# Optimization experiments

Measured on AMD Instinct MI355X. Metric: run time of the kernel, lower is better.

Reference implementation:

```python
import jax, jax.numpy as jnp
import numpy as np

EPS = 1e-5
M = 8          # num_modules
NUM_LAYERS = 4


def gumbel_softmax(logits, u, tau):
    g = -jnp.log(-jnp.log(jnp.clip(u, 1e-10, 1.0 - 1e-7)))
    return jax.nn.softmax((logits + g) / tau, axis=-1)


def batchnorm(x, gamma, beta):
    # training-mode BN over batch axis 0; x: [B, ...], gamma/beta broadcast over trailing dims
    mean = jnp.mean(x, axis=0, keepdims=True)
    var = jnp.mean(jnp.square(x - mean), axis=0, keepdims=True)  # biased var, as torch BN
    return (x - mean) * jax.lax.rsqrt(var + EPS) * gamma + beta


def setup_inputs() -> dict:
    key = jax.random.key(0)
    ks = jax.random.split(key, 32)
    B = 16384
    d = {}
    d['x'] = jax.random.normal(ks[0], (B, 128), jnp.float32)
    d['embedding_input'] = jax.random.normal(ks[1], (B, 128), jnp.float32)
    d['u_sel'] = jax.random.uniform(ks[2], (B, NUM_LAYERS - 1, M, M), jnp.float32)
    d['u_final'] = jax.random.uniform(ks[3], (B, M), jnp.float32)
    shapes = [('base_W0', (128, 400)), ('base_b0', (400,)), ('base_W1', (400, 256)), ('base_b1', (256,)),
              ('em_W0', (128, 400)), ('em_b0', (400,)),
              ('gat_W0', (400, 256)), ('gat_b0', (256,)), ('gat_W1', (256, 256)), ('gat_b1', (256,)),
              ('sel_W', (3, 256, 64)), ('sel_b', (3, 64)), ('selF_W', (256, 8)), ('selF_b', (8,)),
              ('cond_W', (3, 64, 256)), ('cond_b', (3, 256)),
              ('mod_W', (8, 256, 256)), ('mod_b', (8, 256)),
              ('last_W', (256, 18)), ('last_b', (18,))]
    for i, (name, sh) in enumerate(shapes):
        fan_in = sh[-2] if len(sh) >= 2 else sh[-1]
        d[name] = jax.random.normal(ks[4 + i], sh, jnp.float32) / np.sqrt(fan_in)
    d['bn1_g'] = jnp.ones((8, 256), jnp.float32)
    d['bn1_b'] = jnp.zeros((8, 256), jnp.float32)
    d['bn2_g'] = jnp.ones((8, 256), jnp.float32)
    d['bn2_b'] = jnp.zeros((8, 256), jnp.float32)
    return d


def forward(x, embedding_input, u_sel, u_final,
            base_W0, base_b0, base_W1, base_b1, em_W0, em_b0,
            gat_W0, gat_b0, gat_W1, gat_b1,
            sel_W, sel_b, selF_W, selF_b, cond_W, cond_b,
            mod_W, mod_b, bn1_g, bn1_b, bn2_g, bn2_b, last_W, last_b):
    relu = jax.nn.relu
    # base MLP (last activation is identity)
    h = relu(x @ base_W0 + base_b0)
    out = h @ base_W1 + base_b1                       # [B, 256]
    # embedding base (single layer, identity last activation)
    emb = embedding_input @ em_W0 + em_b0             # [B, 400]
    # gating fcs: activation THEN fc, per source loop
    emb = relu(emb) @ gat_W0 + gat_b0
    emb = relu(emb) @ gat_W1 + gat_b1                 # [B, 256]

    # routing logits (stochastic branch, tau = select_temp = 1.0)
    select_input = relu(emb)
    gsels = []
    for i in range(NUM_LAYERS - 1):
        logit = jnp.tanh(select_input @ sel_W[i] + sel_b[i])       # [B, 64]
        sraw = logit.reshape(logit.shape[0], M, M)                  # [B, M, M]
        gsels.append(gumbel_softmax(sraw, u_sel[:, i], 1.0))
        select_input = relu((logit @ cond_W[i] + cond_b[i]) * emb)
    final_select = gumbel_softmax(select_input @ selF_W + selF_b, u_final, 1.0)  # [B, M]
    # selects were insert(0, ...)'d in torch -> consumed in reversed order
    selects = gsels[::-1]

    # layer-0 expert modules: BN -> Linear -> BN (only layers[0] is used in forward)
    mean = jnp.mean(out, axis=0, keepdims=True)
    var = jnp.mean(jnp.square(out - mean), axis=0, keepdims=True)
    xhat = (out - mean) * jax.lax.rsqrt(var + EPS)                  # shared normalization
    t = xhat[:, None, :] * bn1_g + bn1_b                            # [B, M, 256] per-module affine
    h = jnp.einsum('bmd,mdh->bmh', t, mod_W) + mod_b                # [B, M, 256]
    prev = batchnorm(h, bn2_g, bn2_b)                               # [B, M, 256]

    # cascade: weighted combination + relu per layer
    for l in range(NUM_LAYERS - 1):
        prev = relu(jnp.einsum('bmk,bkh->bmh', selects[l], prev))
    out = jnp.einsum('bm,bmh->bh', final_select, prev)              # [B, 256]
    return out @ last_W + last_b                                    # [B, 18]


def reference(x, embedding_input, u_sel, u_final,
              base_W0, base_b0, base_W1, base_b1, em_W0, em_b0,
              gat_W0, gat_b0, gat_W1, gat_b1,
              sel_W, sel_b, selF_W, selF_b, cond_W, cond_b,
              mod_W, mod_b, bn1_g, bn1_b, bn2_g, bn2_b, last_W, last_b):
    return forward(x, embedding_input, u_sel, u_final,
                   base_W0, base_b0, base_W1, base_b1, em_W0, em_b0,
                   gat_W0, gat_b0, gat_W1, gat_b1,
                   sel_W, sel_b, selF_W, selF_b, cond_W, cond_b,
                   mod_W, mod_b, bn1_g, bn1_b, bn2_g, bn2_b, last_W, last_b)
```

## Files before the change

kernel.cpp:

```cpp
#include <hip/hip_runtime.h>
#include <math.h>


typedef short bf16x8 __attribute__((ext_vector_type(8)));
typedef float f32x4 __attribute__((ext_vector_type(4)));

__device__ __forceinline__ unsigned short f2bf(float f) {
  unsigned u = __float_as_uint(f);
  u += 0x7fffu + ((u >> 16) & 1u);
  return (unsigned short)(u >> 16);
}
__device__ __forceinline__ float bf2f(unsigned short h) {
  return __uint_as_float(((unsigned)h) << 16);
}
__device__ __forceinline__ unsigned pack2(float a, float b) {
  return ((unsigned)f2bf(b) << 16) | f2bf(a);
}
__device__ __forceinline__ void gload_lds16(const void* g, void* l) {
  __builtin_amdgcn_global_load_lds(
      (const __attribute__((address_space(1))) unsigned int*)g,
      (__attribute__((address_space(3))) unsigned int*)l, 16, 0, 0);
}
__device__ __forceinline__ bf16x8 relu_bf8(bf16x8 v) {
  bf16x8 r;
  #pragma unroll
  for (int j = 0; j < 8; ++j) r[j] = v[j] > 0 ? v[j] : (short)0;
  return r;
}

#define EPI_NONE  0
#define EPI_RELU  1
#define EPI_STATS 4

__global__ __launch_bounds__(256) void prep_all(
    const float* __restrict__ base_W0, const float* __restrict__ em_W0,
    const float* __restrict__ base_W1, const float* __restrict__ gat_W0,
    const float* __restrict__ gat_W1, const float* __restrict__ sel_W,
    const float* __restrict__ cond_W, const float* __restrict__ last_W,
    const float* __restrict__ selF_W,
    unsigned short* __restrict__ W0t, unsigned short* __restrict__ emW0t,
    unsigned short* __restrict__ W1t, unsigned short* __restrict__ g0t,
    unsigned short* __restrict__ g1t, unsigned short* __restrict__ selWt,
    unsigned short* __restrict__ condWt, unsigned short* __restrict__ lastWt,
    unsigned short* __restrict__ selFt, float* __restrict__ stats)
{
  __shared__ float t[32][33];
  int bid = blockIdx.x;
  const int tid = threadIdx.x;
  const int tx = tid & 31, ty = tid >> 5;

  if (bid < 496) {
    const float* src; unsigned short* dst; int K, N, KP, gx, local;
    if (bid < 64)       { src = base_W0; dst = W0t;   K = 128; N = 400; KP = 128; gx = 4;  local = bid; }
    else if (bid < 128) { src = em_W0;   dst = emW0t; K = 128; N = 400; KP = 128; gx = 4;  local = bid - 64; }
    else if (bid < 232) { src = base_W1; dst = W1t;   K = 400; N = 256; KP = 416; gx = 13; local = bid - 128; }
    else if (bid < 336) { src = gat_W0;  dst = g0t;   K = 400; N = 256; KP = 416; gx = 13; local = bid - 232; }
    else if (bid < 400) { src = gat_W1;  dst = g1t;   K = 256; N = 256; KP = 256; gx = 8;  local = bid - 336; }
    else if (bid < 448) {
      const int i = (bid - 400) / 16;
      src = sel_W + i * 16384; dst = selWt + i * 16384;
      K = 256; N = 64; KP = 256; gx = 8; local = (bid - 400) % 16;
    } else {
      const int i = (bid - 448) / 16;
      src = cond_W + i * 16384; dst = condWt + i * 16384;
      K = 64; N = 256; KP = 64; gx = 2; local = (bid - 448) % 16;
    }
    const int k0 = (local % gx) * 32, n0 = (local / gx) * 32;
    #pragma unroll
    for (int p = 0; p < 4; ++p) {
      const int k = k0 + ty + p * 8;
      t[ty + p * 8][tx] = (k < K && n0 + tx < N) ? src[(size_t)k * N + n0 + tx] : 0.f;
    }
    __syncthreads();
    #pragma unroll
    for (int p = 0; p < 4; ++p) {
      const int n = n0 + ty + p * 8;
      dst[(size_t)n * KP + k0 + tx] = f2bf(t[tx][ty + p * 8]);
    }
    return;
  }
  bid -= 496;

  if (bid < 8) {
    const int k0 = bid * 32;
    #pragma unroll
    for (int p = 0; p < 4; ++p)
      t[ty + p * 8][tx] = (tx < 18) ? last_W[(size_t)(k0 + ty + p * 8) * 18 + tx] : 0.f;
    __syncthreads();
    #pragma unroll
    for (int p = 0; p < 4; ++p) {
      const int n = ty + p * 8;
      lastWt[(size_t)n * 256 + k0 + tx] = f2bf(t[tx][n]);
      lastWt[(size_t)(n + 32) * 256 + k0 + tx] = 0;
    }
    return;
  }
  bid -= 8;

  if (bid == 0) {
    const int k = tid;
    #pragma unroll
    for (int j = 0; j < 8; ++j) selFt[j * 256 + k] = f2bf(selF_W[k * 8 + j]);
    #pragma unroll
    for (int j = 8; j < 16; ++j) selFt[j * 256 + k] = 0;
    return;
  }

  for (int i = tid; i < 4608; i += 256) stats[i] = 0.f;
}

__global__ __launch_bounds__(256) void gemm_w0(
    const float* __restrict__ Ax, const float* __restrict__ Ae,
    const unsigned short* __restrict__ Wx, const unsigned short* __restrict__ We,
    const float* __restrict__ bx, const float* __restrict__ be,
    unsigned short* __restrict__ Cx, unsigned short* __restrict__ Ce)
{
  __shared__ unsigned short As[128 * 32];
  __shared__ unsigned short Bs[128 * 32];
  const float* Ap = blockIdx.z ? Ae : Ax;
  const unsigned short* Wp = blockIdx.z ? We : Wx;
  const float* bp = blockIdx.z ? be : bx;
  unsigned short* Cp = blockIdx.z ? Ce : Cx;
  const int row0 = blockIdx.y * 128;
  const int n0 = blockIdx.x * 128;
  const int tid = threadIdx.x;
  const int wid = tid >> 6, lane = tid & 63;
  const int wr = wid >> 1, wc = wid & 1;
  const int arow = tid >> 2, kcol = (tid & 3) * 8;
  const int lr = lane & 15, lk = (lane >> 4) * 8;
  const int lrow = (lane >> 4) * 4;

  f32x4 acc[4][4] = {};
  for (int k0 = 0; k0 < 128; k0 += 32) {
    {
      const float4* s1 = reinterpret_cast<const float4*>(
          Ap + (size_t)(row0 + arow) * 128 + k0 + kcol);
      uint4 w1 = {pack2(s1[0].x, s1[0].y), pack2(s1[0].z, s1[0].w),
                  pack2(s1[1].x, s1[1].y), pack2(s1[1].z, s1[1].w)};
      *reinterpret_cast<uint4*>(&As[arow * 32 + kcol]) = w1;
      const float4* s2 = reinterpret_cast<const float4*>(
          Ap + (size_t)(row0 + 64 + arow) * 128 + k0 + kcol);
      uint4 w2 = {pack2(s2[0].x, s2[0].y), pack2(s2[0].z, s2[0].w),
                  pack2(s2[1].x, s2[1].y), pack2(s2[1].z, s2[1].w)};
      *reinterpret_cast<uint4*>(&As[(64 + arow) * 32 + kcol]) = w2;
    }
    gload_lds16(Wp + (size_t)(n0 + arow) * 128 + k0 + kcol, (char*)Bs + tid * 16);
    gload_lds16(Wp + (size_t)(n0 + 64 + arow) * 128 + k0 + kcol,
                (char*)Bs + 4096 + tid * 16);
    __syncthreads();
    bf16x8 a[4], b[4];
    #pragma unroll
    for (int i = 0; i < 4; ++i)
      a[i] = *reinterpret_cast<const bf16x8*>(&As[(wr * 64 + i * 16 + lr) * 32 + lk]);
    #pragma unroll
    for (int j = 0; j < 4; ++j)
      b[j] = *reinterpret_cast<const bf16x8*>(&Bs[(wc * 64 + j * 16 + lr) * 32 + lk]);
    #pragma unroll
    for (int i = 0; i < 4; ++i)
      #pragma unroll
      for (int j = 0; j < 4; ++j)
        acc[i][j] = __builtin_amdgcn_mfma_f32_16x16x32_bf16(a[i], b[j], acc[i][j], 0, 0, 0);
    __syncthreads();
  }
  #pragma unroll
  for (int j = 0; j < 4; ++j) {
    const int col = n0 + wc * 64 + j * 16 + lr;
    if (col >= 416) continue;
    const bool real = col < 400;
    const float bv = real ? bp[col] : 0.f;
    #pragma unroll
    for (int i = 0; i < 4; ++i) {
      #pragma unroll
      for (int r = 0; r < 4; ++r) {
        const int row = row0 + wr * 64 + i * 16 + lrow + r;
        float v = real ? fmaxf(acc[i][j][r] + bv, 0.f) : 0.f;
        Cp[(size_t)row * 416 + col] = f2bf(v);
      }
    }
  }
}

__global__ __launch_bounds__(256) void gemm_mid(
    const unsigned short* __restrict__ A0, const unsigned short* __restrict__ W0,
    const float* __restrict__ b0, unsigned short* __restrict__ C0,
    const unsigned short* __restrict__ A1, const unsigned short* __restrict__ W1,
    const float* __restrict__ b1, unsigned short* __restrict__ C1,
    float* __restrict__ sum, float* __restrict__ sumsq)
{
  __shared__ unsigned short As[128 * 32];
  __shared__ unsigned short Bs[64 * 32];
  const bool z1 = blockIdx.z != 0;
  const unsigned short* A = z1 ? A1 : A0;
  const unsigned short* Wt = z1 ? W1 : W0;
  const float* bias = z1 ? b1 : b0;
  unsigned short* C = z1 ? C1 : C0;
  const int row0 = blockIdx.y * 128;
  const int n0 = blockIdx.x * 64;
  const int tid = threadIdx.x;
  const int wid = tid >> 6, lane = tid & 63;
  const int arow = tid >> 2, kcol = (tid & 3) * 8;
  const int lr = lane & 15, lk = (lane >> 4) * 8;
  const int lrow = (lane >> 4) * 4;

  f32x4 acc[2][4] = {};
  for (int k0 = 0; k0 < 416; k0 += 32) {
    gload_lds16(A + (size_t)(row0 + arow) * 416 + k0 + kcol, (char*)As + tid * 16);
    gload_lds16(A + (size_t)(row0 + 64 + arow) * 416 + k0 + kcol, (char*)As + 4096 + tid * 16);
    gload_lds16(Wt + (size_t)(n0 + arow) * 416 + k0 + kcol, (char*)Bs + tid * 16);
    __syncthreads();
    bf16x8 a[2], b[4];
    #pragma unroll
    for (int i = 0; i < 2; ++i)
      a[i] = *reinterpret_cast<const bf16x8*>(&As[(wid * 32 + i * 16 + lr) * 32 + lk]);
    #pragma unroll
    for (int j = 0; j < 4; ++j)
      b[j] = *reinterpret_cast<const bf16x8*>(&Bs[(j * 16 + lr) * 32 + lk]);
    #pragma unroll
    for (int i = 0; i < 2; ++i)
      #pragma unroll
      for (int j = 0; j < 4; ++j)
        acc[i][j] = __builtin_amdgcn_mfma_f32_16x16x32_bf16(a[i], b[j], acc[i][j], 0, 0, 0);
    __syncthreads();
  }
  #pragma unroll
  for (int j = 0; j < 4; ++j) {
    const int col = n0 + j * 16 + lr;
    const float bv = bias[col];
    float s = 0.f, q = 0.f;
    #pragma unroll
    for (int i = 0; i < 2; ++i) {
      #pragma unroll
      for (int r = 0; r < 4; ++r) {
        const int row = row0 + wid * 32 + i * 16 + lrow + r;
        float v = acc[i][j][r] + bv;
        if (z1) v = fmaxf(v, 0.f);
        const unsigned short hv = f2bf(v);
        C[(size_t)row * 256 + col] = hv;
        if (!z1) {
          const float vr = bf2f(hv);
          s += vr;
          q = fmaf(vr, vr, q);
        }
      }
    }
    if (!z1) {
      s += __shfl_xor(s, 16); s += __shfl_xor(s, 32);
      q += __shfl_xor(q, 16); q += __shfl_xor(q, 32);
      if (lane < 16) {
        atomicAdd(&sum[col], s);
        atomicAdd(&sumsq[col], q);
      }
    }
  }
}

template<int BN, int WM, int WN, int EPI, bool RELU_A>
__global__ __launch_bounds__(256) void gemm_bf16(
    const unsigned short* __restrict__ A, int AS,
    const unsigned short* __restrict__ Wt, const float* __restrict__ bias,
    unsigned short* __restrict__ C, int CS, int Nreal, int NP, int K,
    const unsigned short* __restrict__ emb,
    float* __restrict__ sum, float* __restrict__ sumsq)
{
  constexpr int FRAG_M = 128 / WM / 16;
  constexpr int FRAG_N = BN / WN / 16;
  __shared__ unsigned short As[128 * 32];
  __shared__ unsigned short Bs[BN * 32];
  const int row0 = blockIdx.y * 128;
  const int n0 = blockIdx.x * BN;
  const int tid = threadIdx.x;
  const int wid = tid >> 6, lane = tid & 63;
  const int wr = wid / WN, wc = wid % WN;
  const int arow = tid >> 2;
  const int kcol = (tid & 3) * 8;
  const int lr = lane & 15, lk = (lane >> 4) * 8;
  const int lrow = (lane >> 4) * 4;

  f32x4 acc[FRAG_M][FRAG_N] = {};
  for (int k0 = 0; k0 < K; k0 += 32) {
    gload_lds16(A + (size_t)(row0 + arow) * AS + k0 + kcol, (char*)As + tid * 16);
    gload_lds16(A + (size_t)(row0 + 64 + arow) * AS + k0 + kcol, (char*)As + 4096 + tid * 16);
    gload_lds16(Wt + (size_t)(n0 + arow) * K + k0 + kcol, (char*)Bs + tid * 16);
    if constexpr (BN == 128)
      gload_lds16(Wt + (size_t)(n0 + 64 + arow) * K + k0 + kcol, (char*)Bs + 4096 + tid * 16);
    __syncthreads();
    bf16x8 a[FRAG_M], b[FRAG_N];
    #pragma unroll
    for (int i = 0; i < FRAG_M; ++i) {
      a[i] = *reinterpret_cast<const bf16x8*>(&As[(wr * (128 / WM) + i * 16 + lr) * 32 + lk]);
      if (RELU_A) a[i] = relu_bf8(a[i]);
    }
    #pragma unroll
    for (int j = 0; j < FRAG_N; ++j)
      b[j] = *reinterpret_cast<const bf16x8*>(&Bs[(wc * (BN / WN) + j * 16 + lr) * 32 + lk]);
    #pragma unroll
    for (int i = 0; i < FRAG_M; ++i)
      #pragma unroll
      for (int j = 0; j < FRAG_N; ++j)
        acc[i][j] = __builtin_amdgcn_mfma_f32_16x16x32_bf16(a[i], b[j], acc[i][j], 0, 0, 0);
    __syncthreads();
  }
  #pragma unroll
  for (int j = 0; j < FRAG_N; ++j) {
    const int col = n0 + wc * (BN / WN) + j * 16 + lr;
    if (col >= NP) continue;
    const bool real = col < Nreal;
    const float bv = real ? bias[col] : 0.f;
    float s = 0.f, q = 0.f;
    #pragma unroll
    for (int i = 0; i < FRAG_M; ++i) {
      #pragma unroll
      for (int r = 0; r < 4; ++r) {
        const int row = row0 + wr * (128 / WM) + i * 16 + lrow + r;
        float v = acc[i][j][r] + bv;
        if (EPI == EPI_RELU) v = fmaxf(v, 0.f);
        if (!real) v = 0.f;
        const unsigned short hv = f2bf(v);
        C[(size_t)row * CS + col] = hv;
        if (EPI == EPI_STATS) {
          const float vr = bf2f(hv);
          s += vr;
          q = fmaf(vr, vr, q);
        }
      }
    }
    if (EPI == EPI_STATS) {
      s += __shfl_xor(s, 16); s += __shfl_xor(s, 32);
      q += __shfl_xor(q, 16); q += __shfl_xor(q, 32);
      if (lane < 16) {
        atomicAdd(&sum[col], s);
        atomicAdd(&sumsq[col], q);
      }
    }
  }
}

__global__ __launch_bounds__(256) void gemm_mod(
    const unsigned short* __restrict__ A,
    const unsigned short* __restrict__ Wt,
    const float* __restrict__ bias, unsigned short* __restrict__ C,
    float* __restrict__ sum, float* __restrict__ sumsq)
{
  __shared__ unsigned short As[128 * 32];
  __shared__ unsigned short Bs[128 * 32];
  const int lin = blockIdx.x;
  const int swz = (lin & 7) * 256 + (lin >> 3);
  const int row0 = (swz >> 4) * 128;
  const int n0 = (swz & 15) * 128;
  const int tid = threadIdx.x;
  const int wid = tid >> 6, lane = tid & 63;
  const int wr = wid >> 1, wc = wid & 1;
  const int arow = tid >> 2;
  const int kcol = (tid & 3) * 8;
  const int lr = lane & 15, lk = (lane >> 4) * 8;
  const int lrow = (lane >> 4) * 4;

  f32x4 acc[4][4] = {};
  for (int k0 = 0; k0 < 256; k0 += 32) {
    gload_lds16(A + (size_t)(row0 + arow) * 256 + k0 + kcol, (char*)As + tid * 16);
    gload_lds16(A + (size_t)(row0 + 64 + arow) * 256 + k0 + kcol, (char*)As + 4096 + tid * 16);
    gload_lds16(Wt + (size_t)(n0 + arow) * 256 + k0 + kcol, (char*)Bs + tid * 16);
    gload_lds16(Wt + (size_t)(n0 + 64 + arow) * 256 + k0 + kcol, (char*)Bs + 4096 + tid * 16);
    __syncthreads();
    bf16x8 a[4], b[4];
    #pragma unroll
    for (int i = 0; i < 4; ++i)
      a[i] = *reinterpret_cast<const bf16x8*>(&As[(wr * 64 + i * 16 + lr) * 32 + lk]);
    #pragma unroll
    for (int j = 0; j < 4; ++j)
      b[j] = *reinterpret_cast<const bf16x8*>(&Bs[(wc * 64 + j * 16 + lr) * 32 + lk]);
    #pragma unroll
    for (int i = 0; i < 4; ++i)
      #pragma unroll
      for (int j = 0; j < 4; ++j)
        acc[i][j] = __builtin_amdgcn_mfma_f32_16x16x32_bf16(a[i], b[j], acc[i][j], 0, 0, 0);
    __syncthreads();
  }
  #pragma unroll
  for (int j = 0; j < 4; ++j) {
    const int col = n0 + wc * 64 + j * 16 + lr;
    const float bv = bias[col];
    float s = 0.f, q = 0.f;
    #pragma unroll
    for (int i = 0; i < 4; ++i) {
      #pragma unroll
      for (int r = 0; r < 4; ++r) {
        const int row = row0 + wr * 64 + i * 16 + lrow + r;
        const unsigned short hv = f2bf(acc[i][j][r] + bv);
        C[(size_t)row * 2048 + col] = hv;
        const float vr = bf2f(hv);
        s += vr;
        q = fmaf(vr, vr, q);
      }
    }
    s += __shfl_xor(s, 16); s += __shfl_xor(s, 32);
    q += __shfl_xor(q, 16); q += __shfl_xor(q, 32);
    if (lane < 16) {
      atomicAdd(&sum[col], s);
      atomicAdd(&sumsq[col], q);
    }
  }
}

template<bool RELU_A>
__global__ __launch_bounds__(256) void fused_select(
    const unsigned short* __restrict__ A, const unsigned short* __restrict__ selWt,
    const float* __restrict__ selb, const unsigned short* __restrict__ condWt,
    const float* __restrict__ condb, const unsigned short* __restrict__ emb,
    const float* __restrict__ u, int u_off,
    float* __restrict__ gs, unsigned short* __restrict__ siout)
{
  __shared__ unsigned short As[128 * 32];
  __shared__ unsigned short Bs[64 * 32];
  __shared__ unsigned short Ls[128 * 72];
  const int tid = threadIdx.x;
  const int wid = tid >> 6, lane = tid & 63;
  const int lr = lane & 15, hi = lane >> 4;
  const int lk = hi * 8;
  const int row0 = blockIdx.x * 128;
  const int arow = tid >> 2, kcol = (tid & 3) * 8;

  {
    f32x4 acc[2][4] = {};
    for (int k0 = 0; k0 < 256; k0 += 32) {
      gload_lds16(A + (size_t)(row0 + arow) * 256 + k0 + kcol, (char*)As + tid * 16);
      gload_lds16(A + (size_t)(row0 + 64 + arow) * 256 + k0 + kcol, (char*)As + 4096 + tid * 16);
      gload_lds16(selWt + (size_t)arow * 256 + k0 + kcol, (char*)Bs + tid * 16);
      __syncthreads();
      bf16x8 a[2], b[4];
      #pragma unroll
      for (int i = 0; i < 2; ++i) {
        a[i] = *reinterpret_cast<const bf16x8*>(&As[(wid * 32 + i * 16 + lr) * 32 + lk]);
        if (RELU_A) a[i] = relu_bf8(a[i]);
      }
      #pragma unroll
      for (int j = 0; j < 4; ++j)
        b[j] = *reinterpret_cast<const bf16x8*>(&Bs[(j * 16 + lr) * 32 + lk]);
      #pragma unroll
      for (int i = 0; i < 2; ++i)
        #pragma unroll
        for (int j = 0; j < 4; ++j)
          acc[i][j] = __builtin_amdgcn_mfma_f32_16x16x32_bf16(a[i], b[j], acc[i][j], 0, 0, 0);
      __syncthreads();
    }
    #pragma unroll
    for (int j = 0; j < 4; ++j) {
      const int col = j * 16 + lr;
      const float bv = selb[col];
      #pragma unroll
      for (int i = 0; i < 2; ++i)
        #pragma unroll
        for (int r = 0; r < 4; ++r) {
          const int row = wid * 32 + i * 16 + hi * 4 + r;
          Ls[row * 72 + col] = f2bf(tanhf(acc[i][j][r] + bv));
        }
    }
  }
  __syncthreads();

  #pragma unroll
  for (int p = 0; p < 4; ++p) {
    const int pair = p * 256 + tid;
    const int bl = pair >> 3, mm = pair & 7;
    const int bg = row0 + bl;
    float v[8];
    #pragma unroll
    for (int jj = 0; jj < 8; ++jj) v[jj] = bf2f(Ls[bl * 72 + mm * 8 + jj]);
    const float* up = u + (size_t)bg * 192 + u_off + mm * 8;
    #pragma unroll
    for (int jj = 0; jj < 8; ++jj) {
      const float uu = fminf(fmaxf(up[jj], 1e-10f), 0.9999999f);
      v[jj] -= logf(-logf(uu));
    }
    float mx = v[0];
    #pragma unroll
    for (int jj = 1; jj < 8; ++jj) mx = fmaxf(mx, v[jj]);
    float s = 0.f;
    #pragma unroll
    for (int jj = 0; jj < 8; ++jj) { v[jj] = expf(v[jj] - mx); s += v[jj]; }
    const float inv = 1.f / s;
    float* op = gs + (size_t)bg * 64 + mm * 8;
    #pragma unroll
    for (int jj = 0; jj < 8; ++jj) op[jj] = v[jj] * inv;
  }

  {
    const int wr2 = wid >> 1, wc2 = wid & 1;
    f32x4 acc2[4][8] = {};
    #pragma unroll
    for (int kq = 0; kq < 2; ++kq) {
      const int k0 = kq * 32;
      bf16x8 a2[4];
      #pragma unroll
      for (int i = 0; i < 4; ++i)
        a2[i] = *reinterpret_cast<const bf16x8*>(
            &Ls[(wr2 * 64 + i * 16 + lr) * 72 + k0 + hi * 8]);
      #pragma unroll
      for (int j = 0; j < 8; ++j) {
        const bf16x8 b2 = *reinterpret_cast<const bf16x8*>(
            condWt + (size_t)(wc2 * 128 + j * 16 + lr) * 64 + k0 + hi * 8);
        #pragma unroll
        for (int i = 0; i < 4; ++i)
          acc2[i][j] = __builtin_amdgcn_mfma_f32_16x16x32_bf16(a2[i], b2, acc2[i][j], 0, 0, 0);
      }
    }
    #pragma unroll
    for (int j = 0; j < 8; ++j) {
      const int col = wc2 * 128 + j * 16 + lr;
      const float bv = condb[col];
      #pragma unroll
      for (int i = 0; i < 4; ++i)
        #pragma unroll
        for (int r = 0; r < 4; ++r) {
          const int row = row0 + wr2 * 64 + i * 16 + hi * 4 + r;
          float vv = (acc2[i][j][r] + bv) * bf2f(emb[(size_t)row * 256 + col]);
          siout[(size_t)row * 256 + col] = f2bf(fmaxf(vv, 0.f));
        }
    }
  }
}

__global__ __launch_bounds__(256) void gemm_fsel(
    const unsigned short* __restrict__ A, const unsigned short* __restrict__ Wt,
    const float* __restrict__ bias, const float* __restrict__ u,
    float* __restrict__ fs)
{
  __shared__ unsigned short As[128 * 32];
  __shared__ unsigned short Bs[16 * 32];
  const int row0 = blockIdx.y * 128;
  const int tid = threadIdx.x;
  const int wid = tid >> 6, lane = tid & 63;
  const int arow = tid >> 2, kcol = (tid & 3) * 8;
  const int lr = lane & 15, hi = lane >> 4;
  const int lk = hi * 8;

  f32x4 acc[2] = {};
  for (int k0 = 0; k0 < 256; k0 += 32) {
    gload_lds16(A + (size_t)(row0 + arow) * 256 + k0 + kcol, (char*)As + tid * 16);
    gload_lds16(A + (size_t)(row0 + 64 + arow) * 256 + k0 + kcol, (char*)As + 4096 + tid * 16);
    if (wid == 0)
      gload_lds16(Wt + (size_t)(lane >> 2) * 256 + k0 + (lane & 3) * 8, (char*)Bs + lane * 16);
    __syncthreads();
    bf16x8 a[2];
    #pragma unroll
    for (int i = 0; i < 2; ++i)
      a[i] = *reinterpret_cast<const bf16x8*>(&As[(wid * 32 + i * 16 + lr) * 32 + lk]);
    const bf16x8 b = *reinterpret_cast<const bf16x8*>(&Bs[lr * 32 + lk]);
    #pragma unroll
    for (int i = 0; i < 2; ++i)
      acc[i] = __builtin_amdgcn_mfma_f32_16x16x32_bf16(a[i], b, acc[i], 0, 0, 0);
    __syncthreads();
  }
  const float bv = (lr < 8) ? bias[lr] : 0.f;
  #pragma unroll
  for (int i = 0; i < 2; ++i) {
    #pragma unroll
    for (int r = 0; r < 4; ++r) {
      const int row = row0 + wid * 32 + i * 16 + hi * 4 + r;
      float v = acc[i][r] + bv;
      if (lr < 8) {
        const float uu = fminf(fmaxf(u[(size_t)row * 8 + lr], 1e-10f), 0.9999999f);
        v -= logf(-logf(uu));
      }
      float mx = v;
      mx = fmaxf(mx, __shfl_xor(mx, 1));
      mx = fmaxf(mx, __shfl_xor(mx, 2));
      mx = fmaxf(mx, __shfl_xor(mx, 4));
      const float e = expf(v - mx);
      float ssum = e;
      ssum += __shfl_xor(ssum, 1);
      ssum += __shfl_xor(ssum, 2);
      ssum += __shfl_xor(ssum, 4);
      if (lr < 8) fs[(size_t)row * 8 + lr] = e / ssum;
    }
  }
}

__global__ __launch_bounds__(256) void fold_modw_all(
    const float* __restrict__ W, const float* __restrict__ g1,
    const float* __restrict__ b1, const float* __restrict__ modb,
    const float* __restrict__ sum1, const float* __restrict__ sumsq1,
    unsigned short* __restrict__ Wt, float* __restrict__ bias2)
{
  const float invB = 1.f / 16384.f;
  if (blockIdx.z == 8) {
    if (blockIdx.y != 0) return;
    const int m = blockIdx.x, h = threadIdx.x;
    float acc = modb[m * 256 + h];
    for (int d = 0; d < 256; ++d) {
      const float mean = sum1[d] * invB;
      const float var = sumsq1[d] * invB - mean * mean;
      const float r = rsqrtf(var + 1e-5f);
      const float c = b1[m * 256 + d] - mean * r * g1[m * 256 + d];
      acc = fmaf(c, W[((size_t)m * 256 + d) * 256 + h], acc);
    }
    bias2[m * 256 + h] = acc;
    return;
  }
  __shared__ float t[32][33];
  const int m = blockIdx.z, d0 = blockIdx.y * 32, h0 = blockIdx.x * 32;
  const int tx = threadIdx.x & 31, ty = threadIdx.x >> 5;
  #pragma unroll
  for (int p = 0; p < 4; ++p) {
    const int d = d0 + ty + p * 8;
    const float mean = sum1[d] * invB;
    const float var = sumsq1[d] * invB - mean * mean;
    const float r = rsqrtf(var + 1e-5f);
    t[ty + p * 8][tx] = W[((size_t)m * 256 + d) * 256 + h0 + tx] * r * g1[m * 256 + d];
  }
  __syncthreads();
  #pragma unroll
  for (int p = 0; p < 4; ++p) {
    const int h = h0 + ty + p * 8;
    Wt[((size_t)m * 256 + h) * 256 + d0 + tx] = f2bf(t[tx][ty + p * 8]);
  }
}

__global__ void finalize_bn2(const float* __restrict__ sum, const float* __restrict__ sumsq,
                             const float* __restrict__ g, const float* __restrict__ b,
                             float* __restrict__ scale, float* __restrict__ shift)
{
  const int i = blockIdx.x * 256 + threadIdx.x;
  const float invB = 1.f / 16384.f;
  const float m = sum[i] * invB;
  const float v = sumsq[i] * invB - m * m;
  const float r = rsqrtf(v + 1e-5f);
  const float sc = r * g[i];
  scale[i] = sc;
  shift[i] = b[i] - m * sc;
}

__global__ __launch_bounds__(256) void final_cascade(
    const unsigned short* __restrict__ H, const float* __restrict__ scale2,
    const float* __restrict__ shift2, const float* __restrict__ gs0,
    const float* __restrict__ gs1, const float* __restrict__ gs2,
    const float* __restrict__ fs, unsigned short* __restrict__ ovec)
{
  const int wave = threadIdx.x >> 6, lane = threadIdx.x & 63;
  const int b = __builtin_amdgcn_readfirstlane(blockIdx.x * 4 + wave);
  const int c0 = lane << 2;

  float prev[8][4];
  #pragma unroll
  for (int m = 0; m < 8; ++m) {
    const int gc = m * 256 + c0;
    const ushort4 h = *reinterpret_cast<const ushort4*>(&H[(size_t)b * 2048 + gc]);
    const float4 sc = *reinterpret_cast<const float4*>(&scale2[gc]);
    const float4 sh = *reinterpret_cast<const float4*>(&shift2[gc]);
    prev[m][0] = bf2f(h.x) * sc.x + sh.x;
    prev[m][1] = bf2f(h.y) * sc.y + sh.y;
    prev[m][2] = bf2f(h.z) * sc.z + sh.z;
    prev[m][3] = bf2f(h.w) * sc.w + sh.w;
  }

  const float* sel0 = gs2 + (size_t)b * 64;
  const float* sel1 = gs1 + (size_t)b * 64;
  const float* sel2 = gs0 + (size_t)b * 64;
  #pragma unroll
  for (int l = 0; l < 3; ++l) {
    const float* sp = (l == 0) ? sel0 : (l == 1) ? sel1 : sel2;
    float nw[8][4];
    #pragma unroll
    for (int m = 0; m < 8; ++m) {
      float a0 = 0.f, a1 = 0.f, a2 = 0.f, a3 = 0.f;
      #pragma unroll
      for (int k = 0; k < 8; ++k) {
        const float s = sp[m * 8 + k];
        a0 = fmaf(s, prev[k][0], a0);
        a1 = fmaf(s, prev[k][1], a1);
        a2 = fmaf(s, prev[k][2], a2);
        a3 = fmaf(s, prev[k][3], a3);
      }
      nw[m][0] = fmaxf(a0, 0.f); nw[m][1] = fmaxf(a1, 0.f);
      nw[m][2] = fmaxf(a2, 0.f); nw[m][3] = fmaxf(a3, 0.f);
    }
    #pragma unroll
    for (int m = 0; m < 8; ++m)
      #pragma unroll
      for (int c = 0; c < 4; ++c)
        prev[m][c] = nw[m][c];
  }

  const float* fp = fs + (size_t)b * 8;
  float ov[4] = {0.f, 0.f, 0.f, 0.f};
  #pragma unroll
  for (int m = 0; m < 8; ++m) {
    const float s = fp[m];
    ov[0] = fmaf(s, prev[m][0], ov[0]);
    ov[1] = fmaf(s, prev[m][1], ov[1]);
    ov[2] = fmaf(s, prev[m][2], ov[2]);
    ov[3] = fmaf(s, prev[m][3], ov[3]);
  }
  ushort4 o;
  o.x = f2bf(ov[0]); o.y = f2bf(ov[1]); o.z = f2bf(ov[2]); o.w = f2bf(ov[3]);
  *reinterpret_cast<ushort4*>(&ovec[(size_t)b * 256 + c0]) = o;
}

__global__ __launch_bounds__(256) void gemm_last(
    const unsigned short* __restrict__ A, const unsigned short* __restrict__ Wt,
    const float* __restrict__ bias, float* __restrict__ out)
{
  __shared__ unsigned short As[128 * 32];
  __shared__ unsigned short Bs[64 * 32];
  const int row0 = blockIdx.y * 128;
  const int tid = threadIdx.x;
  const int wid = tid >> 6, lane = tid & 63;
  const int arow = tid >> 2;
  const int kcol = (tid & 3) * 8;
  const int lr = lane & 15, lk = (lane >> 4) * 8;
  const int lrow = (lane >> 4) * 4;

  f32x4 acc[2][4] = {};
  for (int k0 = 0; k0 < 256; k0 += 32) {
    gload_lds16(A + (size_t)(row0 + arow) * 256 + k0 + kcol, (char*)As + tid * 16);
    gload_lds16(A + (size_t)(row0 + 64 + arow) * 256 + k0 + kcol, (char*)As + 4096 + tid * 16);
    gload_lds16(Wt + (size_t)arow * 256 + k0 + kcol, (char*)Bs + tid * 16);
    __syncthreads();
    bf16x8 a[2], b[4];
    #pragma unroll
    for (int i = 0; i < 2; ++i)
      a[i] = *reinterpret_cast<const bf16x8*>(&As[(wid * 32 + i * 16 + lr) * 32 + lk]);
    #pragma unroll
    for (int j = 0; j < 4; ++j)
      b[j] = *reinterpret_cast<const bf16x8*>(&Bs[(j * 16 + lr) * 32 + lk]);
    #pragma unroll
    for (int i = 0; i < 2; ++i)
      #pragma unroll
      for (int j = 0; j < 4; ++j)
        acc[i][j] = __builtin_amdgcn_mfma_f32_16x16x32_bf16(a[i], b[j], acc[i][j], 0, 0, 0);
    __syncthreads();
  }
  #pragma unroll
  for (int j = 0; j < 2; ++j) {
    const int col = j * 16 + lr;
    if (col >= 18) continue;
    const float bv = bias[col];
    #pragma unroll
    for (int i = 0; i < 2; ++i) {
      #pragma unroll
      for (int r = 0; r < 4; ++r) {
        const int row = row0 + wid * 32 + i * 16 + lrow + r;
        out[(size_t)row * 18 + col] = acc[i][j][r] + bv;
      }
    }
  }
}

extern "C" void kernel_launch(void* const* d_in, const int* in_sizes, int n_in,
                              void* d_out, int out_size, void* d_ws, size_t ws_size,
                              hipStream_t stream)
{
  (void)in_sizes; (void)n_in; (void)out_size; (void)ws_size;
  const float* x       = (const float*)d_in[0];
  const float* embi    = (const float*)d_in[1];
  const float* u_sel   = (const float*)d_in[2];
  const float* u_fin   = (const float*)d_in[3];
  const float* base_W0 = (const float*)d_in[4];
  const float* base_b0 = (const float*)d_in[5];
  const float* base_W1 = (const float*)d_in[6];
  const float* base_b1 = (const float*)d_in[7];
  const float* em_W0   = (const float*)d_in[8];
  const float* em_b0   = (const float*)d_in[9];
  const float* gat_W0  = (const float*)d_in[10];
  const float* gat_b0  = (const float*)d_in[11];
  const float* gat_W1  = (const float*)d_in[12];
  const float* gat_b1  = (const float*)d_in[13];
  const float* sel_W   = (const float*)d_in[14];
  const float* sel_b   = (const float*)d_in[15];
  const float* selF_W  = (const float*)d_in[16];
  const float* selF_b  = (const float*)d_in[17];
  const float* cond_W  = (const float*)d_in[18];
  const float* cond_b  = (const float*)d_in[19];
  const float* mod_W   = (const float*)d_in[20];
  const float* mod_b   = (const float*)d_in[21];
  const float* last_W  = (const float*)d_in[22];
  const float* last_b  = (const float*)d_in[23];
  const float* bn1_g   = (const float*)d_in[24];
  const float* bn1_b   = (const float*)d_in[25];
  const float* bn2_g   = (const float*)d_in[26];
  const float* bn2_b   = (const float*)d_in[27];

  char* WSB = (char*)d_ws;
  unsigned short* h_big    = (unsigned short*)(WSB + 0);
  unsigned short* h1e      = (unsigned short*)(WSB + 67108864);
  unsigned short* ovec_bf  = (unsigned short*)(WSB + 67108864);
  unsigned short* h1       = (unsigned short*)(WSB + 81000448);
  unsigned short* emb_bf   = (unsigned short*)(WSB + 103020544);
  unsigned short* si_bf    = (unsigned short*)(WSB + 111409152);
  unsigned short* out_bf   = (unsigned short*)(WSB + 119797760);
  float* gs0   = (float*)(WSB + 130283520);
  float* gs1   = (float*)(WSB + 134477824);
  float* gs2   = (float*)(WSB + 138672128);
  float* bufFs = (float*)(WSB + 142866432);
  unsigned short* W0t   = (unsigned short*)(WSB + 143390720);
  unsigned short* emW0t = (unsigned short*)(WSB + 143521792);
  unsigned short* W1t   = (unsigned short*)(WSB + 143652864);
  unsigned short* g0t   = (unsigned short*)(WSB + 143865856);
  unsigned short* g1t   = (unsigned short*)(WSB + 144078848);
  unsigned short* selWt = (unsigned short*)(WSB + 144209920);
  unsigned short* condWt= (unsigned short*)(WSB + 144308224);
  unsigned short* modWt = (unsigned short*)(WSB + 144406528);
  float* bias2  = (float*)(WSB + 146503680);
  float* stats  = (float*)(WSB + 146511872);
  unsigned short* lastWt = (unsigned short*)(WSB + 146530304);
  float* scale2 = (float*)(WSB + 146563072);
  float* shift2 = (float*)(WSB + 146571264);
  unsigned short* selFt = (unsigned short*)(WSB + 146579456);
  float* sum1   = stats;        float* sumsq1 = stats + 256;
  float* sum2   = stats + 512;  float* sumsq2 = stats + 2560;

  const dim3 blk(256);
  prep_all<<<dim3(506), blk, 0, stream>>>(
      base_W0, em_W0, base_W1, gat_W0, gat_W1, sel_W, cond_W, last_W, selF_W,
      W0t, emW0t, W1t, g0t, g1t, selWt, condWt, lastWt, selFt, stats);

  gemm_w0<<<dim3(4, 128, 2), blk, 0, stream>>>(
      x, embi, W0t, emW0t, base_b0, em_b0, h1, h1e);
  gemm_mid<<<dim3(4, 128, 2), blk, 0, stream>>>(
      h1, W1t, base_b1, out_bf, h1e, g0t, gat_b0, si_bf, sum1, sumsq1);
  gemm_bf16<64, 4, 1, EPI_NONE, false><<<dim3(4, 128), blk, 0, stream>>>(
      si_bf, 256, g1t, gat_b1, emb_bf, 256, 256, 256, 256, nullptr, nullptr, nullptr);
  fused_select<true><<<dim3(128), blk, 0, stream>>>(
      emb_bf, selWt, sel_b, condWt, cond_b, emb_bf, u_sel, 0, gs0, si_bf);
  fused_select<false><<<dim3(128), blk, 0, stream>>>(
      si_bf, selWt + 16384, sel_b + 64, condWt + 16384, cond_b + 256, emb_bf,
      u_sel, 64, gs1, si_bf);
  fused_select<false><<<dim3(128), blk, 0, stream>>>(
      si_bf, selWt + 32768, sel_b + 128, condWt + 32768, cond_b + 512, emb_bf,
      u_sel, 128, gs2, si_bf);
  gemm_fsel<<<dim3(1, 128), blk, 0, stream>>>(si_bf, selFt, selF_b, u_fin, bufFs);
  fold_modw_all<<<dim3(8, 8, 9), blk, 0, stream>>>(
      mod_W, bn1_g, bn1_b, mod_b, sum1, sumsq1, modWt, bias2);
  gemm_mod<<<dim3(2048), blk, 0, stream>>>(out_bf, modWt, bias2, h_big, sum2, sumsq2);
  finalize_bn2<<<dim3(8), blk, 0, stream>>>(sum2, sumsq2, bn2_g, bn2_b, scale2, shift2);
  final_cascade<<<dim3(4096), blk, 0, stream>>>(
      h_big, scale2, shift2, gs0, gs1, gs2, bufFs, ovec_bf);
  gemm_last<<<dim3(1, 128), blk, 0, stream>>>(ovec_bf, lastWt, last_b, (float*)d_out);
}
```

Measured before the change: 247.9 us.

## Permute gemm_mod output columns for vector stores; halve row tiles in small GEMMs

The gemm_mod epilogue now writes each row's four per-lane columns as one packed ushort4 store instead of scattered 2-byte stores. To allow this, the hidden dimension is stored in a permuted order inside each 64-column group. The BN2 finalize and the last_W transpose are remapped so that the permutation cancels out through the cascade. Separately, fused_select, gemm_fsel and gemm_last now use 64-row tiles with 256 blocks instead of 128-row tiles with 128 blocks, to occupy more CUs. The cost is more weight reloads per block and a fragile layout contract spread across several kernels.

```diff
diff --git a/kernel.cpp b/kernel.cpp
--- a/kernel.cpp
+++ b/kernel.cpp
@@ -81,21 +81,18 @@
   }
   bid -= 496;
 
-  if (bid < 8) {
-    const int k0 = bid * 32;
-    #pragma unroll
-    for (int p = 0; p < 4; ++p)
-      t[ty + p * 8][tx] = (tx < 18) ? last_W[(size_t)(k0 + ty + p * 8) * 18 + tx] : 0.f;
-    __syncthreads();
-    #pragma unroll
-    for (int p = 0; p < 4; ++p) {
-      const int n = ty + p * 8;
-      lastWt[(size_t)n * 256 + k0 + tx] = f2bf(t[tx][n]);
-      lastWt[(size_t)(n + 32) * 256 + k0 + tx] = 0;
-    }
+  if (bid == 0) {
+    const int tc = tid;
+    const int g = tc >> 6, t64 = tc & 63;
+    const int pk = g * 64 + (t64 & 15) * 4 + (t64 >> 4);
+    #pragma unroll
+    for (int n = 0; n < 18; ++n)
+      lastWt[n * 256 + pk] = f2bf(last_W[(size_t)tc * 18 + n]);
+    #pragma unroll
+    for (int n = 18; n < 64; ++n) lastWt[n * 256 + pk] = 0;
     return;
   }
-  bid -= 8;
+  bid -= 1;
 
   if (bid == 0) {
     const int k = tid;
@@ -353,7 +350,7 @@
   const int arow = tid >> 2;
   const int kcol = (tid & 3) * 8;
   const int lr = lane & 15, lk = (lane >> 4) * 8;
-  const int lrow = (lane >> 4) * 4;
+  const int hi = lane >> 4;
 
   f32x4 acc[4][4] = {};
   for (int k0 = 0; k0 < 256; k0 += 32) {
@@ -376,28 +373,41 @@
         acc[i][j] = __builtin_amdgcn_mfma_f32_16x16x32_bf16(a[i], b[j], acc[i][j], 0, 0, 0);
     __syncthreads();
   }
+
+  float bv[4];
+  #pragma unroll
+  for (int j = 0; j < 4; ++j) bv[j] = bias[n0 + wc * 64 + j * 16 + lr];
   #pragma unroll
   for (int j = 0; j < 4; ++j) {
-    const int col = n0 + wc * 64 + j * 16 + lr;
-    const float bv = bias[col];
     float s = 0.f, q = 0.f;
     #pragma unroll
-    for (int i = 0; i < 4; ++i) {
+    for (int i = 0; i < 4; ++i)
       #pragma unroll
       for (int r = 0; r < 4; ++r) {
-        const int row = row0 + wr * 64 + i * 16 + lrow + r;
-        const unsigned short hv = f2bf(acc[i][j][r] + bv);
-        C[(size_t)row * 2048 + col] = hv;
-        const float vr = bf2f(hv);
+        const float vr = bf2f(f2bf(acc[i][j][r] + bv[j]));
         s += vr;
         q = fmaf(vr, vr, q);
       }
-    }
     s += __shfl_xor(s, 16); s += __shfl_xor(s, 32);
     q += __shfl_xor(q, 16); q += __shfl_xor(q, 32);
     if (lane < 16) {
-      atomicAdd(&sum[col], s);
-      atomicAdd(&sumsq[col], q);
+      const int pcol = n0 + wc * 64 + lr * 4 + j;
+      atomicAdd(&sum[pcol], s);
+      atomicAdd(&sumsq[pcol], q);
+    }
+  }
+  const int pbase = n0 + wc * 64 + lr * 4;
+  #pragma unroll
+  for (int i = 0; i < 4; ++i) {
+    #pragma unroll
+    for (int r = 0; r < 4; ++r) {
+      const int row = row0 + wr * 64 + i * 16 + hi * 4 + r;
+      ushort4 o;
+      o.x = f2bf(acc[i][0][r] + bv[0]);
+      o.y = f2bf(acc[i][1][r] + bv[1]);
+      o.z = f2bf(acc[i][2][r] + bv[2]);
+      o.w = f2bf(acc[i][3][r] + bv[3]);
+      *reinterpret_cast<ushort4*>(&C[(size_t)row * 2048 + pbase]) = o;
     }
   }
 }
@@ -410,37 +420,29 @@
     const float* __restrict__ u, int u_off,
     float* __restrict__ gs, unsigned short* __restrict__ siout)
 {
-  __shared__ unsigned short As[128 * 32];
+  __shared__ unsigned short As[64 * 32];
   __shared__ unsigned short Bs[64 * 32];
-  __shared__ unsigned short Ls[128 * 72];
+  __shared__ unsigned short Ls[64 * 72];
   const int tid = threadIdx.x;
   const int wid = tid >> 6, lane = tid & 63;
   const int lr = lane & 15, hi = lane >> 4;
   const int lk = hi * 8;
-  const int row0 = blockIdx.x * 128;
+  const int row0 = blockIdx.x * 64;
   const int arow = tid >> 2, kcol = (tid & 3) * 8;
 
   {
-    f32x4 acc[2][4] = {};
+    f32x4 acc[4] = {};
     for (int k0 = 0; k0 < 256; k0 += 32) {
       gload_lds16(A + (size_t)(row0 + arow) * 256 + k0 + kcol, (char*)As + tid * 16);
-      gload_lds16(A + (size_t)(row0 + 64 + arow) * 256 + k0 + kcol, (char*)As + 4096 + tid * 16);
       gload_lds16(selWt + (size_t)arow * 256 + k0 + kcol, (char*)Bs + tid * 16);
       __syncthreads();
-      bf16x8 a[2], b[4];
-      #pragma unroll
-      for (int i = 0; i < 2; ++i) {
-        a[i] = *reinterpret_cast<const bf16x8*>(&As[(wid * 32 + i * 16 + lr) * 32 + lk]);
-        if (RELU_A) a[i] = relu_bf8(a[i]);
-      }
-      #pragma unroll
-      for (int j = 0; j < 4; ++j)
-        b[j] = *reinterpret_cast<const bf16x8*>(&Bs[(j * 16 + lr) * 32 + lk]);
-      #pragma unroll
-      for (int i = 0; i < 2; ++i)
-        #pragma unroll
-        for (int j = 0; j < 4; ++j)
-          acc[i][j] = __builtin_amdgcn_mfma_f32_16x16x32_bf16(a[i], b[j], acc[i][j], 0, 0, 0);
+      bf16x8 a = *reinterpret_cast<const bf16x8*>(&As[(wid * 16 + lr) * 32 + lk]);
+      if (RELU_A) a = relu_bf8(a);
+      #pragma unroll
+      for (int j = 0; j < 4; ++j) {
+        const bf16x8 b = *reinterpret_cast<const bf16x8*>(&Bs[(j * 16 + lr) * 32 + lk]);
+        acc[j] = __builtin_amdgcn_mfma_f32_16x16x32_bf16(a, b, acc[j], 0, 0, 0);
+      }
       __syncthreads();
     }
     #pragma unroll
@@ -448,18 +450,16 @@
       const int col = j * 16 + lr;
       const float bv = selb[col];
       #pragma unroll
-      for (int i = 0; i < 2; ++i)
-        #pragma unroll
-        for (int r = 0; r < 4; ++r) {
-          const int row = wid * 32 + i * 16 + hi * 4 + r;
-          Ls[row * 72 + col] = f2bf(tanhf(acc[i][j][r] + bv));
-        }
+      for (int r = 0; r < 4; ++r) {
+        const int row = wid * 16 + hi * 4 + r;
+        Ls[row * 72 + col] = f2bf(tanhf(acc[j][r] + bv));
+      }
     }
   }
   __syncthreads();
 
   #pragma unroll
-  for (int p = 0; p < 4; ++p) {
+  for (int p = 0; p < 2; ++p) {
     const int pair = p * 256 + tid;
     const int bl = pair >> 3, mm = pair & 7;
     const int bg = row0 + bl;
@@ -486,21 +486,21 @@
 
   {
     const int wr2 = wid >> 1, wc2 = wid & 1;
-    f32x4 acc2[4][8] = {};
+    f32x4 acc2[2][8] = {};
     #pragma unroll
     for (int kq = 0; kq < 2; ++kq) {
       const int k0 = kq * 32;
-      bf16x8 a2[4];
-      #pragma unroll
-      for (int i = 0; i < 4; ++i)
+      bf16x8 a2[2];
+      #pragma unroll
+      for (int i = 0; i < 2; ++i)
         a2[i] = *reinterpret_cast<const bf16x8*>(
-            &Ls[(wr2 * 64 + i * 16 + lr) * 72 + k0 + hi * 8]);
+            &Ls[(wr2 * 32 + i * 16 + lr) * 72 + k0 + hi * 8]);
       #pragma unroll
       for (int j = 0; j < 8; ++j) {
         const bf16x8 b2 = *reinterpret_cast<const bf16x8*>(
             condWt + (size_t)(wc2 * 128 + j * 16 + lr) * 64 + k0 + hi * 8);
         #pragma unroll
-        for (int i = 0; i < 4; ++i)
+        for (int i = 0; i < 2; ++i)
           acc2[i][j] = __builtin_amdgcn_mfma_f32_16x16x32_bf16(a2[i], b2, acc2[i][j], 0, 0, 0);
       }
     }
@@ -509,10 +509,10 @@
       const int col = wc2 * 128 + j * 16 + lr;
       const float bv = condb[col];
       #pragma unroll
-      for (int i = 0; i < 4; ++i)
+      for (int i = 0; i < 2; ++i)
         #pragma unroll
         for (int r = 0; r < 4; ++r) {
-          const int row = row0 + wr2 * 64 + i * 16 + hi * 4 + r;
+          const int row = row0 + wr2 * 32 + i * 16 + hi * 4 + r;
           float vv = (acc2[i][j][r] + bv) * bf2f(emb[(size_t)row * 256 + col]);
           siout[(size_t)row * 256 + col] = f2bf(fmaxf(vv, 0.f));
         }
@@ -525,54 +525,45 @@
     const float* __restrict__ bias, const float* __restrict__ u,
     float* __restrict__ fs)
 {
-  __shared__ unsigned short As[128 * 32];
+  __shared__ unsigned short As[64 * 32];
   __shared__ unsigned short Bs[16 * 32];
-  const int row0 = blockIdx.y * 128;
+  const int row0 = blockIdx.x * 64;
   const int tid = threadIdx.x;
   const int wid = tid >> 6, lane = tid & 63;
   const int arow = tid >> 2, kcol = (tid & 3) * 8;
   const int lr = lane & 15, hi = lane >> 4;
   const int lk = hi * 8;
 
-  f32x4 acc[2] = {};
+  f32x4 acc = {};
   for (int k0 = 0; k0 < 256; k0 += 32) {
     gload_lds16(A + (size_t)(row0 + arow) * 256 + k0 + kcol, (char*)As + tid * 16);
-    gload_lds16(A + (size_t)(row0 + 64 + arow) * 256 + k0 + kcol, (char*)As + 4096 + tid * 16);
     if (wid == 0)
       gload_lds16(Wt + (size_t)(lane >> 2) * 256 + k0 + (lane & 3) * 8, (char*)Bs + lane * 16);
     __syncthreads();
-    bf16x8 a[2];
-    #pragma unroll
-    for (int i = 0; i < 2; ++i)
-      a[i] = *reinterpret_cast<const bf16x8*>(&As[(wid * 32 + i * 16 + lr) * 32 + lk]);
+    const bf16x8 a = *reinterpret_cast<const bf16x8*>(&As[(wid * 16 + lr) * 32 + lk]);
     const bf16x8 b = *reinterpret_cast<const bf16x8*>(&Bs[lr * 32 + lk]);
-    #pragma unroll
-    for (int i = 0; i < 2; ++i)
-      acc[i] = __builtin_amdgcn_mfma_f32_16x16x32_bf16(a[i], b, acc[i], 0, 0, 0);
+    acc = __builtin_amdgcn_mfma_f32_16x16x32_bf16(a, b, acc, 0, 0, 0);
     __syncthreads();
   }
   const float bv = (lr < 8) ? bias[lr] : 0.f;
   #pragma unroll
-  for (int i = 0; i < 2; ++i) {
-    #pragma unroll
-    for (int r = 0; r < 4; ++r) {
-      const int row = row0 + wid * 32 + i * 16 + hi * 4 + r;
-      float v = acc[i][r] + bv;
-      if (lr < 8) {
-        const float uu = fminf(fmaxf(u[(size_t)row * 8 + lr], 1e-10f), 0.9999999f);
-        v -= logf(-logf(uu));
-      }
-      float mx = v;
-      mx = fmaxf(mx, __shfl_xor(mx, 1));
-      mx = fmaxf(mx, __shfl_xor(mx, 2));
-      mx = fmaxf(mx, __shfl_xor(mx, 4));
-      const float e = expf(v - mx);
-      float ssum = e;
-      ssum += __shfl_xor(ssum, 1);
-      ssum += __shfl_xor(ssum, 2);
-      ssum += __shfl_xor(ssum, 4);
-      if (lr < 8) fs[(size_t)row * 8 + lr] = e / ssum;
-    }
+  for (int r = 0; r < 4; ++r) {
+    const int row = row0 + wid * 16 + hi * 4 + r;
+    float v = acc[r] + bv;
+    if (lr < 8) {
+      const float uu = fminf(fmaxf(u[(size_t)row * 8 + lr], 1e-10f), 0.9999999f);
+      v -= logf(-logf(uu));
+    }
+    float mx = v;
+    mx = fmaxf(mx, __shfl_xor(mx, 1));
+    mx = fmaxf(mx, __shfl_xor(mx, 2));
+    mx = fmaxf(mx, __shfl_xor(mx, 4));
+    const float e = expf(v - mx);
+    float ssum = e;
+    ssum += __shfl_xor(ssum, 1);
+    ssum += __shfl_xor(ssum, 2);
+    ssum += __shfl_xor(ssum, 4);
+    if (lr < 8) fs[(size_t)row * 8 + lr] = e / ssum;
   }
 }
 
@@ -621,13 +612,15 @@
                              float* __restrict__ scale, float* __restrict__ shift)
 {
   const int i = blockIdx.x * 256 + threadIdx.x;
+  const int pos64 = i & 63;
+  const int tc = (i & ~63) | ((pos64 & 3) * 16 + (pos64 >> 2));
   const float invB = 1.f / 16384.f;
   const float m = sum[i] * invB;
   const float v = sumsq[i] * invB - m * m;
   const float r = rsqrtf(v + 1e-5f);
-  const float sc = r * g[i];
+  const float sc = r * g[tc];
   scale[i] = sc;
-  shift[i] = b[i] - m * sc;
+  shift[i] = b[tc] - m * sc;
 }
 
 __global__ __launch_bounds__(256) void final_cascade(
@@ -700,34 +693,26 @@
     const unsigned short* __restrict__ A, const unsigned short* __restrict__ Wt,
     const float* __restrict__ bias, float* __restrict__ out)
 {
-  __shared__ unsigned short As[128 * 32];
+  __shared__ unsigned short As[64 * 32];
   __shared__ unsigned short Bs[64 * 32];
-  const int row0 = blockIdx.y * 128;
+  const int row0 = blockIdx.x * 64;
   const int tid = threadIdx.x;
   const int wid = tid >> 6, lane = tid & 63;
-  const int arow = tid >> 2;
-  const int kcol = (tid & 3) * 8;
-  const int lr = lane & 15, lk = (lane >> 4) * 8;
-  const int lrow = (lane >> 4) * 4;
-
-  f32x4 acc[2][4] = {};
+  const int arow = tid >> 2, kcol = (tid & 3) * 8;
+  const int lr = lane & 15, hi = lane >> 4;
+  const int lk = hi * 8;
+
+  f32x4 acc[4] = {};
   for (int k0 = 0; k0 < 256; k0 += 32) {
     gload_lds16(A + (size_t)(row0 + arow) * 256 + k0 + kcol, (char*)As + tid * 16);
-    gload_lds16(A + (size_t)(row0 + 64 + arow) * 256 + k0 + kcol, (char*)As + 4096 + tid * 16);
     gload_lds16(Wt + (size_t)arow * 256 + k0 + kcol, (char*)Bs + tid * 16);
     __syncthreads();
-    bf16x8 a[2], b[4];
-    #pragma unroll
-    for (int i = 0; i < 2; ++i)
-      a[i] = *reinterpret_cast<const bf16x8*>(&As[(wid * 32 + i * 16 + lr) * 32 + lk]);
-    #pragma unroll
-    for (int j = 0; j < 4; ++j)
-      b[j] = *reinterpret_cast<const bf16x8*>(&Bs[(j * 16 + lr) * 32 + lk]);
-    #pragma unroll
-    for (int i = 0; i < 2; ++i)
-      #pragma unroll
-      for (int j = 0; j < 4; ++j)
-        acc[i][j] = __builtin_amdgcn_mfma_f32_16x16x32_bf16(a[i], b[j], acc[i][j], 0, 0, 0);
+    const bf16x8 a = *reinterpret_cast<const bf16x8*>(&As[(wid * 16 + lr) * 32 + lk]);
+    #pragma unroll
+    for (int j = 0; j < 4; ++j) {
+      const bf16x8 b = *reinterpret_cast<const bf16x8*>(&Bs[(j * 16 + lr) * 32 + lk]);
+      acc[j] = __builtin_amdgcn_mfma_f32_16x16x32_bf16(a, b, acc[j], 0, 0, 0);
+    }
     __syncthreads();
   }
   #pragma unroll
@@ -736,12 +721,9 @@
     if (col >= 18) continue;
     const float bv = bias[col];
     #pragma unroll
-    for (int i = 0; i < 2; ++i) {
-      #pragma unroll
-      for (int r = 0; r < 4; ++r) {
-        const int row = row0 + wid * 32 + i * 16 + lrow + r;
-        out[(size_t)row * 18 + col] = acc[i][j][r] + bv;
-      }
+    for (int r = 0; r < 4; ++r) {
+      const int row = row0 + wid * 16 + hi * 4 + r;
+      out[(size_t)row * 18 + col] = acc[j][r] + bv;
     }
   }
 }
@@ -810,7 +792,7 @@
   float* sum2   = stats + 512;  float* sumsq2 = stats + 2560;
 
   const dim3 blk(256);
-  prep_all<<<dim3(506), blk, 0, stream>>>(
+  prep_all<<<dim3(499), blk, 0, stream>>>(
       base_W0, em_W0, base_W1, gat_W0, gat_W1, sel_W, cond_W, last_W, selF_W,
       W0t, emW0t, W1t, g0t, g1t, selWt, condWt, lastWt, selFt, stats);
 
@@ -820,20 +802,20 @@
       h1, W1t, base_b1, out_bf, h1e, g0t, gat_b0, si_bf, sum1, sumsq1);
   gemm_bf16<64, 4, 1, EPI_NONE, false><<<dim3(4, 128), blk, 0, stream>>>(
       si_bf, 256, g1t, gat_b1, emb_bf, 256, 256, 256, 256, nullptr, nullptr, nullptr);
-  fused_select<true><<<dim3(128), blk, 0, stream>>>(
+  fused_select<true><<<dim3(256), blk, 0, stream>>>(
       emb_bf, selWt, sel_b, condWt, cond_b, emb_bf, u_sel, 0, gs0, si_bf);
-  fused_select<false><<<dim3(128), blk, 0, stream>>>(
+  fused_select<false><<<dim3(256), blk, 0, stream>>>(
       si_bf, selWt + 16384, sel_b + 64, condWt + 16384, cond_b + 256, emb_bf,
       u_sel, 64, gs1, si_bf);
-  fused_select<false><<<dim3(128), blk, 0, stream>>>(
+  fused_select<false><<<dim3(256), blk, 0, stream>>>(
       si_bf, selWt + 32768, sel_b + 128, condWt + 32768, cond_b + 512, emb_bf,
       u_sel, 128, gs2, si_bf);
-  gemm_fsel<<<dim3(1, 128), blk, 0, stream>>>(si_bf, selFt, selF_b, u_fin, bufFs);
+  gemm_fsel<<<dim3(256), blk, 0, stream>>>(si_bf, selFt, selF_b, u_fin, bufFs);
   fold_modw_all<<<dim3(8, 8, 9), blk, 0, stream>>>(
       mod_W, bn1_g, bn1_b, mod_b, sum1, sumsq1, modWt, bias2);
   gemm_mod<<<dim3(2048), blk, 0, stream>>>(out_bf, modWt, bias2, h_big, sum2, sumsq2);
   finalize_bn2<<<dim3(8), blk, 0, stream>>>(sum2, sumsq2, bn2_g, bn2_b, scale2, shift2);
   final_cascade<<<dim3(4096), blk, 0, stream>>>(
       h_big, scale2, shift2, gs0, gs1, gs2, bufFs, ovec_bf);
-  gemm_last<<<dim3(1, 128), blk, 0, stream>>>(ovec_bf, lastWt, last_b, (float*)d_out);
-}
+  gemm_last<<<dim3(256), blk, 0, stream>>>(ovec_bf, lastWt, last_b, (float*)d_out);
+}
```

New measurement: 256.2 us. 1.03x slower.
